# Performance work log

Measured on AMD Instinct MI355X. Metric: run time of the kernel, lower is better.

The kernel has to match this reference:

```python
import jax, jax.numpy as jnp
import numpy as np

# Shapes hard-coded by the original module
B, C1, C2, S, K, H, E = 128, 128, 14, 14, 3, 256, 2  # batch, chan-split, chan-split, spatial, kernel, hidden, expand


def setup_inputs() -> dict:
    key = jax.random.key(0)
    k1, k2, k3 = jax.random.split(key, 3)
    x = jax.random.normal(k1, (B, C1 * C2, S), dtype=jnp.float32)
    w0 = jax.random.normal(k2, (H, E), dtype=jnp.float32)        # weights[0]
    w1 = jax.random.normal(k3, (C1, K, H), dtype=jnp.float32)    # weights[1]
    return {"x": x, "w0": w0, "w1": w1, "shift": 1}


def reference(x, w0, w1, shift):
    # reshape to (B, C1, C2, S); original torch treats it as (B, 1792, 14, 1)
    xr = x.reshape(B, C1, C2, S)
    # unfold((3,1), padding=(1,0)): 1D im2col along the S (=14) axis
    xp = jnp.pad(xr, ((0, 0), (0, 0), (0, 0), (1, 1)))
    # patches[b, j, n, i, m] = xp[b, j, n, m + i]  -> (B, C1, C2, K, S)
    patches = jnp.stack([xp[..., k:k + S] for k in range(K)], axis=3)
    # einsum 'ljnmi,jik->lnmk' (torch had m,i swapped via permute; fold it in)
    t4 = jnp.einsum('ljnim,jik->lnmk', patches, w1)   # (B, C2, S, H)
    # einsum 'kmlj,ji->kmlji': outer product with w0 along a new expand dim
    t5 = t4[..., None] * w0                            # (B, C2, S, H, E)
    t5 = jnp.roll(t5, shift, axis=1)                   # cyclic shift over C2
    t6 = jnp.transpose(t5, (0, 2, 3, 1, 4)).reshape(B, S, H, C2 * E)
    t6 = jnp.roll(t6, shift, axis=3)                   # cyclic shift over merged (C2*E)
    t6 = t6.reshape(B, S, H, C2, E).sum(axis=4)        # (B, S, H, C2)
    return jnp.transpose(t6, (0, 2, 3, 1))             # (B, H, C2, S) = (128, 256, 14, 14)
```

## Files before the change

kernel.cpp:

```cpp
#include <hip/hip_runtime.h>
#include <hip/hip_bf16.h>
#include <math.h>

#define B_   128
#define C1_  128
#define C2_  14
#define S_   14
#define K_   3
#define H_   256
#define E_   2

#define HT   64
#define NT   4
#define XR    121
#define XCHUNK (XR * 64)
#define BT_OFF 15488
#define LDS_SZ 40064
#define CROW 116

typedef unsigned short u16;
typedef unsigned int   u32;
typedef __attribute__((ext_vector_type(8))) short bf16x8;
typedef __attribute__((ext_vector_type(4))) float f32x4;

#define ASYNC16(g, l) __builtin_amdgcn_global_load_lds(                        \
    (const __attribute__((address_space(1))) void*)(g),                        \
    (__attribute__((address_space(3))) void*)(l), 16, 0, 0)

__device__ __forceinline__ u16 f2bf(float f) {
    u32 u = __float_as_uint(f);
    return (u16)((u + 0x7FFF + ((u >> 16) & 1)) >> 16);
}

__device__ __forceinline__ int decode_shift(const int* p) {
    int a = p[0];
    if (a >= -100 && a <= 100 && a != 0) return a;
    float f = __int_as_float(a);
    if (f >= -100.f && f <= 100.f && f == truncf(f) && f != 0.f) return (int)f;
    long long bits = ((long long)p[1] << 32) | (unsigned int)a;
    double d = __longlong_as_double(bits);
    if (d >= -100.0 && d <= 100.0 && d == trunc(d) && d != 0.0) return (int)d;
    return a;
}

__global__ __launch_bounds__(512) void cvt_kernel(const float* __restrict__ x,
                                                  const float* __restrict__ w1,
                                                  u16* __restrict__ xg,
                                                  u16* __restrict__ wg) {
    const int blk = blockIdx.x;
    const int t   = threadIdx.x;
    if (blk < 256) {
        __shared__ u16 xl[64 * 200];
        const int b  = blk >> 1;
        const int hf = blk & 1;
        const float4* src = (const float4*)(x + (size_t)(b * C1_ + hf * 64) * 196);
#pragma unroll
        for (int i = 0; i < 7; ++i) {
            int q = t + 512 * i;
            if (q < 3136) {
                float4 v = src[q];
                int c1l = q / 49, f4 = q - c1l * 49;
                uint2 w;
                w.x = (u32)f2bf(v.x) | ((u32)f2bf(v.y) << 16);
                w.y = (u32)f2bf(v.z) | ((u32)f2bf(v.w) << 16);
                *(uint2*)&xl[c1l * 200 + f4 * 4] = w;
            }
        }
        __syncthreads();
        u16* dst = xg + (size_t)(b * 2 + hf) * (2 * XCHUNK);
#pragma unroll
        for (int i = 0; i < 4; ++i) {
            int idx = t + 512 * i;
            if (idx < 1936) {
                int half = idx / 968, rem = idx - half * 968;
                int rr = rem >> 3, o = rem & 7;
                int c2l = rr / 15, p = rr - c2l * 15;
                uint4 val = make_uint4(0, 0, 0, 0);
                if (p != 0 && rr != 120) {
                    int c2g = half * 7 + c2l; if (c2g >= 14) c2g -= 14;
                    int cs = c2g * 14 + p - 1;
                    u16 v[8];
#pragma unroll
                    for (int j = 0; j < 8; ++j) v[j] = xl[(o * 8 + j) * 200 + cs];
                    val.x = (u32)v[0] | ((u32)v[1] << 16);
                    val.y = (u32)v[2] | ((u32)v[3] << 16);
                    val.z = (u32)v[4] | ((u32)v[5] << 16);
                    val.w = (u32)v[6] | ((u32)v[7] << 16);
                }
                int op = o ^ (rr & 7);
                *(uint4*)&dst[(half * XR + rr) * 64 + op * 8] = val;
            }
        }
    } else {
        int q = (blk - 256) * 512 + t;
        float4 v = ((const float4*)w1)[q];
        int i0 = q * 4;
        int c1 = i0 / 768;
        int kk = (i0 - c1 * 768) >> 8;
        int h0 = i0 & 255;
        int hf = c1 >> 6, c1l = c1 & 63;
        int cb0 = c1l >> 3, j = c1l & 7;
        u16 b4[4] = { f2bf(v.x), f2bf(v.y), f2bf(v.z), f2bf(v.w) };
#pragma unroll
        for (int d = 0; d < 4; ++d) {
            int h = h0 + d, g = h >> 6, hl = h & 63;
            int cb = cb0 ^ (hl & 7);
            wg[(size_t)((g * 2 + hf) * 64 + hl) * 192 + kk * 64 + cb * 8 + j] = b4[d];
        }
    }
}

__global__ __launch_bounds__(256, 4) void fused_kernel(const u16* __restrict__ xg,
                                                       const float* __restrict__ w0,
                                                       const u16* __restrict__ wg,
                                                       const int* __restrict__ shift_p,
                                                       float* __restrict__ out) {
    __shared__ __align__(16) char lds[LDS_SZ];
    float* Cl = (float*)lds;

    const int raw  = blockIdx.x;
    const int u    = raw & 255;
    const int g    = raw >> 8;
    const int b    = u >> 1;
    const int half = u & 1;
    const int c0   = half * 7;
    const int h0   = g * HT;
    const int t    = threadIdx.x;
    const int wave = t >> 6;
    const int lane = t & 63;
    const int quad = lane >> 4;
    const int l15  = lane & 15;
    const int wbase = t & ~63;

    int rb[2]; bool vm[2];
#pragma unroll
    for (int mi = 0; mi < 2; ++mi) {
        int mt = wave + 4 * mi;
        vm[mi] = (mt < 7);
        int m = mt * 16 + l15;
        if (m > 111) m = 111;
        rb[mi] = m + m / 14;
    }

    f32x4 acc[2][NT];
#pragma unroll
    for (int i = 0; i < 2; ++i)
#pragma unroll
        for (int j = 0; j < NT; ++j) acc[i][j] = (f32x4){0.f, 0.f, 0.f, 0.f};

    for (int hf = 0; hf < 2; ++hf) {
        if (hf) __syncthreads();
        const uint4* xs = (const uint4*)(xg + ((size_t)(b * 2 + hf) * 2 + half) * XCHUNK);
        const uint4* bs = (const uint4*)(wg + (size_t)(g * 2 + hf) * (64 * 192));
#pragma unroll
        for (int i = 0; i < 4; ++i) {
            int idx = t + 256 * i;
            if (idx < 968)
                ASYNC16(xs + idx, lds + (size_t)(256 * i + wbase) * 16);
        }
#pragma unroll
        for (int i = 0; i < 6; ++i)
            ASYNC16(bs + 256 * i + t, lds + BT_OFF + (size_t)(256 * i + wbase) * 16);
        __syncthreads();

#pragma unroll
        for (int tt = 0; tt < 6; ++tt) {
            const int kk  = tt >> 1;
            const int cbl = (tt & 1) * 4 + quad;
            const int bsw = (cbl ^ (l15 & 7)) << 4;
            bf16x8 bfr[NT];
#pragma unroll
            for (int nc = 0; nc < NT; ++nc)
                bfr[nc] = *(const bf16x8*)(lds + BT_OFF +
                            (nc * 16 + l15) * 384 + kk * 128 + bsw);
#pragma unroll
            for (int mi = 0; mi < 2; ++mi) {
                if (vm[mi]) {
                    int row = rb[mi] + kk;
                    bf16x8 af = *(const bf16x8*)(lds + row * 128 +
                                 ((cbl ^ (row & 7)) << 4));
#pragma unroll
                    for (int nc = 0; nc < NT; ++nc)
                        acc[mi][nc] = __builtin_amdgcn_mfma_f32_16x16x32_bf16(
                            af, bfr[nc], acc[mi][nc], 0, 0, 0);
                }
            }
        }
    }

    __syncthreads();
#pragma unroll
    for (int mi = 0; mi < 2; ++mi) {
        int mt = wave + 4 * mi;
        if (vm[mi]) {
#pragma unroll
            for (int nc = 0; nc < NT; ++nc) {
                int hl = nc * 16 + l15;
                *(f32x4*)&Cl[hl * CROW + mt * 16 + quad * 4] = acc[mi][nc];
            }
        }
    }
    __syncthreads();

    const int shift = decode_shift(shift_p);
    const int hl = t >> 2, sub = t & 3;
    const int h = h0 + hl;
    int aE[2], epE[2];
#pragma unroll
    for (int e = 0; e < 2; ++e) {
        int q = (e - shift) % 28; if (q < 0) q += 28;
        int np0 = q >> 1; epE[e] = q & 1;
        int c2p0 = (np0 - shift) % 14; if (c2p0 < 0) c2p0 += 14;
        aE[e] = (14 - c2p0) % 14;
    }
    int diff = aE[0] - aE[1]; if (diff < 0) diff += 14;
    int A = (diff == 13) ? aE[1] : aE[0];
    int base0 = ((A - aE[0] + 14) % 14) * 14;
    int base1 = ((A - aE[1] + 14) % 14) * 14;
    float wv0 = w0[h * 2 + epE[0]], wv1 = w0[h * 2 + epE[1]];
    int n0g = c0 + A; if (n0g >= 14) n0g -= 14;
    const int o0 = n0g * 14;
    const float* Crow = &Cl[hl * CROW];
    float* orow = out + (size_t)(b * H_ + h) * 196;
#pragma unroll
    for (int i = 0; i < 13; ++i) {
        int j = sub + 4 * i;
        if (j < 49) {
            int p = 2 * j;
            float v0 = wv0 * Crow[base0 + p]     + wv1 * Crow[base1 + p];
            float v1 = wv0 * Crow[base0 + p + 1] + wv1 * Crow[base1 + p + 1];
            int o = o0 + p; if (o >= 196) o -= 196;
            *(float2*)&orow[o] = make_float2(v0, v1);
        }
    }
}

__global__ __launch_bounds__(256) void t4_fb(const float* __restrict__ x,
                                             const float* __restrict__ w1,
                                             float* __restrict__ t4) {
    __shared__ float xl[C1_][16];
    const int b = blockIdx.x / C2_, c2 = blockIdx.x % C2_, h = threadIdx.x;
    for (int i = h; i < C1_ * S_; i += 256) {
        int c1 = i / S_, s = i % S_;
        xl[c1][s + 1] = x[((size_t)(b * C1_ + c1) * C2_ + c2) * S_ + s];
    }
    if (h < C1_) { xl[h][0] = 0.f; xl[h][15] = 0.f; }
    __syncthreads();
    float acc[S_];
#pragma unroll
    for (int s = 0; s < S_; ++s) acc[s] = 0.f;
    for (int c1 = 0; c1 < C1_; ++c1) {
        float wa = w1[(size_t)(c1 * K_ + 0) * H_ + h];
        float wb = w1[(size_t)(c1 * K_ + 1) * H_ + h];
        float wc = w1[(size_t)(c1 * K_ + 2) * H_ + h];
#pragma unroll
        for (int s = 0; s < S_; ++s)
            acc[s] += wa * xl[c1][s] + wb * xl[c1][s + 1] + wc * xl[c1][s + 2];
    }
    size_t base = ((size_t)(b * H_ + h) * C2_ + c2) * S_;
#pragma unroll
    for (int s = 0; s < S_; ++s) t4[base + s] = acc[s];
}
__global__ __launch_bounds__(224) void out_fb(float* __restrict__ t4,
                                              const float* __restrict__ w0,
                                              const int* __restrict__ shift_p) {
    const int tid = threadIdx.x;
    const int m = tid % S_, hh = tid / S_;
    const int b = blockIdx.x / 16, h = (blockIdx.x % 16) * 16 + hh;
    const int shift = decode_shift(shift_p);
    const size_t colbase = ((size_t)(b * H_ + h) * C2_) * S_ + m;
    float tl[C2_];
#pragma unroll
    for (int c2 = 0; c2 < C2_; ++c2) tl[c2] = t4[colbase + (size_t)c2 * S_];
    const float w0v[2] = { w0[h * 2 + 0], w0[h * 2 + 1] };
    float r[C2_];
#pragma unroll
    for (int n = 0; n < C2_; ++n) {
        float a = 0.f;
#pragma unroll
        for (int e = 0; e < 2; ++e) {
            int q = (2 * n + e - shift) % 28; if (q < 0) q += 28;
            int np = q >> 1, ep = q & 1;
            int c2 = (np - shift) % 14; if (c2 < 0) c2 += 14;
            a += tl[c2] * w0v[ep];
        }
        r[n] = a;
    }
#pragma unroll
    for (int n = 0; n < C2_; ++n) t4[colbase + (size_t)n * S_] = r[n];
}

extern "C" void kernel_launch(void* const* d_in, const int* in_sizes, int n_in,
                              void* d_out, int out_size, void* d_ws, size_t ws_size,
                              hipStream_t stream) {
    const float* x     = (const float*)d_in[0];
    const float* w0    = (const float*)d_in[1];
    const float* w1    = (const float*)d_in[2];
    const int*   shift = (const int*)(n_in > 3 ? d_in[3] : d_in[n_in - 1]);
    for (int i = 0; i < n_in; ++i) {
        int sz = in_sizes[i];
        if (sz == B_ * C1_ * C2_ * S_)      x     = (const float*)d_in[i];
        else if (sz == H_ * E_)             w0    = (const float*)d_in[i];
        else if (sz == C1_ * K_ * H_)       w1    = (const float*)d_in[i];
        else if (sz == 1)                   shift = (const int*)d_in[i];
    }
    float* out = (float*)d_out;

    const size_t NXG = (size_t)B_ * 2 * 2 * XCHUNK;
    const size_t NWG = (size_t)4 * 2 * 64 * 192;
    if (ws_size >= (NXG + NWG) * sizeof(u16)) {
        u16* xg = (u16*)d_ws;
        u16* wg = xg + NXG;
        cvt_kernel<<<304, 512, 0, stream>>>(x, w1, xg, wg);
        fused_kernel<<<1024, 256, 0, stream>>>(xg, w0, wg, shift, out);
    } else {
        t4_fb<<<B_ * C2_, 256, 0, stream>>>(x, w1, out);
        out_fb<<<B_ * 16, 224, 0, stream>>>(out, w0, shift);
    }
}
```

Measured before the change: 87.97 us.

## Load MFMA operands directly from global memory, dropping LDS staging

The fused kernel no longer stages x and weight tiles into LDS with async global-to-LDS copies and barriers. Weights are pre-packed by the conversion kernel into per-lane MFMA fragment order, so each lane issues one contiguous 16-byte global load per fragment. The A operand is read straight from the global x buffer without the XOR swizzle. This removes the LDS traffic, the swizzle arithmetic and the mid-loop barrier, and frees LDS so more blocks can be resident. The cost is that every wave hits global memory or cache directly, with overlapping rows re-read across the three kernel taps, and A-row reads are less coalesced.

```diff
diff --git a/kernel.cpp b/kernel.cpp
--- a/kernel.cpp
+++ b/kernel.cpp
@@ -14,18 +14,12 @@
 #define NT   4
 #define XR    121
 #define XCHUNK (XR * 64)
-#define BT_OFF 15488
-#define LDS_SZ 40064
 #define CROW 116
 
 typedef unsigned short u16;
 typedef unsigned int   u32;
 typedef __attribute__((ext_vector_type(8))) short bf16x8;
 typedef __attribute__((ext_vector_type(4))) float f32x4;
-
-#define ASYNC16(g, l) __builtin_amdgcn_global_load_lds(                        \
-    (const __attribute__((address_space(1))) void*)(g),                        \
-    (__attribute__((address_space(3))) void*)(l), 16, 0, 0)
 
 __device__ __forceinline__ u16 f2bf(float f) {
     u32 u = __float_as_uint(f);
@@ -87,25 +81,25 @@
                     val.z = (u32)v[4] | ((u32)v[5] << 16);
                     val.w = (u32)v[6] | ((u32)v[7] << 16);
                 }
-                int op = o ^ (rr & 7);
-                *(uint4*)&dst[(half * XR + rr) * 64 + op * 8] = val;
+                *(uint4*)&dst[(half * XR + rr) * 64 + o * 8] = val;
             }
         }
     } else {
-        int q = (blk - 256) * 512 + t;
-        float4 v = ((const float4*)w1)[q];
-        int i0 = q * 4;
+        int q4 = (blk - 256) * 512 + t;
+        float4 v = ((const float4*)w1)[q4];
+        int i0 = q4 * 4;
         int c1 = i0 / 768;
         int kk = (i0 - c1 * 768) >> 8;
         int h0 = i0 & 255;
         int hf = c1 >> 6, c1l = c1 & 63;
-        int cb0 = c1l >> 3, j = c1l & 7;
+        int c1h = c1l >> 5, qd = (c1l >> 3) & 3, j = c1l & 7;
+        int kt = hf * 6 + kk * 2 + c1h;
         u16 b4[4] = { f2bf(v.x), f2bf(v.y), f2bf(v.z), f2bf(v.w) };
 #pragma unroll
         for (int d = 0; d < 4; ++d) {
-            int h = h0 + d, g = h >> 6, hl = h & 63;
-            int cb = cb0 ^ (hl & 7);
-            wg[(size_t)((g * 2 + hf) * 64 + hl) * 192 + kk * 64 + cb * 8 + j] = b4[d];
+            int h = h0 + d, g = h >> 6, nc = (h >> 4) & 3, l15 = h & 15;
+            int lane = qd * 16 + l15;
+            wg[((size_t)(((g * 12 + kt) * 4 + nc) * 64 + lane) << 3) + j] = b4[d];
         }
     }
 }
@@ -115,8 +109,7 @@
                                                        const u16* __restrict__ wg,
                                                        const int* __restrict__ shift_p,
                                                        float* __restrict__ out) {
-    __shared__ __align__(16) char lds[LDS_SZ];
-    float* Cl = (float*)lds;
+    __shared__ __align__(16) float Cl[64 * CROW];
 
     const int raw  = blockIdx.x;
     const int u    = raw & 255;
@@ -130,7 +123,6 @@
     const int lane = t & 63;
     const int quad = lane >> 4;
     const int l15  = lane & 15;
-    const int wbase = t & ~63;
 
     int rb[2]; bool vm[2];
 #pragma unroll
@@ -142,48 +134,35 @@
         rb[mi] = m + m / 14;
     }
 
+    const u16* xs0 = xg + ((size_t)(b * 2 + 0) * 2 + half) * XCHUNK;
+    const u16* xs1 = xg + ((size_t)(b * 2 + 1) * 2 + half) * XCHUNK;
+    const bf16x8* wfrag = (const bf16x8*)(wg) + (size_t)g * (12 * 4 * 64) + lane;
+
     f32x4 acc[2][NT];
 #pragma unroll
     for (int i = 0; i < 2; ++i)
 #pragma unroll
         for (int j = 0; j < NT; ++j) acc[i][j] = (f32x4){0.f, 0.f, 0.f, 0.f};
 
-    for (int hf = 0; hf < 2; ++hf) {
-        if (hf) __syncthreads();
-        const uint4* xs = (const uint4*)(xg + ((size_t)(b * 2 + hf) * 2 + half) * XCHUNK);
-        const uint4* bs = (const uint4*)(wg + (size_t)(g * 2 + hf) * (64 * 192));
-#pragma unroll
-        for (int i = 0; i < 4; ++i) {
-            int idx = t + 256 * i;
-            if (idx < 968)
-                ASYNC16(xs + idx, lds + (size_t)(256 * i + wbase) * 16);
-        }
-#pragma unroll
-        for (int i = 0; i < 6; ++i)
-            ASYNC16(bs + 256 * i + t, lds + BT_OFF + (size_t)(256 * i + wbase) * 16);
-        __syncthreads();
-
-#pragma unroll
-        for (int tt = 0; tt < 6; ++tt) {
-            const int kk  = tt >> 1;
-            const int cbl = (tt & 1) * 4 + quad;
-            const int bsw = (cbl ^ (l15 & 7)) << 4;
-            bf16x8 bfr[NT];
-#pragma unroll
-            for (int nc = 0; nc < NT; ++nc)
-                bfr[nc] = *(const bf16x8*)(lds + BT_OFF +
-                            (nc * 16 + l15) * 384 + kk * 128 + bsw);
-#pragma unroll
-            for (int mi = 0; mi < 2; ++mi) {
-                if (vm[mi]) {
-                    int row = rb[mi] + kk;
-                    bf16x8 af = *(const bf16x8*)(lds + row * 128 +
-                                 ((cbl ^ (row & 7)) << 4));
-#pragma unroll
-                    for (int nc = 0; nc < NT; ++nc)
-                        acc[mi][nc] = __builtin_amdgcn_mfma_f32_16x16x32_bf16(
-                            af, bfr[nc], acc[mi][nc], 0, 0, 0);
-                }
+#pragma unroll
+    for (int kt = 0; kt < 12; ++kt) {
+        const int hf  = kt / 6, rem = kt - hf * 6;
+        const int kk  = rem >> 1, c1h = rem & 1;
+        const int coff = c1h * 32 + quad * 8;
+        const u16* xs = hf ? xs1 : xs0;
+        bf16x8 bfr[NT];
+#pragma unroll
+        for (int nc = 0; nc < NT; ++nc)
+            bfr[nc] = wfrag[(kt * 4 + nc) * 64];
+#pragma unroll
+        for (int mi = 0; mi < 2; ++mi) {
+            if (vm[mi]) {
+                int row = rb[mi] + kk;
+                bf16x8 af = *(const bf16x8*)(xs + row * 64 + coff);
+#pragma unroll
+                for (int nc = 0; nc < NT; ++nc)
+                    acc[mi][nc] = __builtin_amdgcn_mfma_f32_16x16x32_bf16(
+                        af, bfr[nc], acc[mi][nc], 0, 0, 0);
             }
         }
     }
@@ -307,7 +286,7 @@
     float* out = (float*)d_out;
 
     const size_t NXG = (size_t)B_ * 2 * 2 * XCHUNK;
-    const size_t NWG = (size_t)4 * 2 * 64 * 192;
+    const size_t NWG = (size_t)4 * 12 * 4 * 64 * 8;
     if (ws_size >= (NXG + NWG) * sizeof(u16)) {
         u16* xg = (u16*)d_ws;
         u16* wg = xg + NXG;
```

After: 98.61 us. +12.1%, slower.
